# Optimization experiments

Hardware: AMD Instinct MI355X
Metric: run time of the kernel (lower is better)

Reference implementation:

```python
import jax, jax.numpy as jnp
import numpy as np

EMBED_DIM = 1024
NUM_HEADS = 16
HEAD_DIM = EMBED_DIM // NUM_HEADS
WINDOW = 256


def setup_inputs() -> dict:
    key = jax.random.key(0)
    ks = jax.random.split(key, 9)
    B, S, E = 4, 4096, EMBED_DIM
    sc = 1.0 / np.sqrt(E)
    return {
        "x": jax.random.normal(ks[0], (B, S, E), jnp.float32),
        "Wq": jax.random.normal(ks[1], (E, E), jnp.float32) * sc,
        "bq": jax.random.normal(ks[2], (E,), jnp.float32) * 0.01,
        "Wk": jax.random.normal(ks[3], (E, E), jnp.float32) * sc,
        "bk": jax.random.normal(ks[4], (E,), jnp.float32) * 0.01,
        "Wv": jax.random.normal(ks[5], (E, E), jnp.float32) * sc,
        "bv": jax.random.normal(ks[6], (E,), jnp.float32) * 0.01,
        "Wo": jax.random.normal(ks[7], (E, E), jnp.float32) * sc,
        "bo": jax.random.normal(ks[8], (E,), jnp.float32) * 0.01,
    }


def reference(x, Wq, bq, Wk, bk, Wv, bv, Wo, bo):
    B, S, E = x.shape
    H, D, W = NUM_HEADS, HEAD_DIM, WINDOW
    NW = S // W  # seq_len chosen divisible by window -> no padding

    def split_heads(t):  # [B,S,E] -> [B,H,NW,W,D]
        return t.reshape(B, S, H, D).transpose(0, 2, 1, 3).reshape(B, H, NW, W, D)

    q = split_heads(x @ Wq + bq)
    k = split_heads(x @ Wk + bk)
    v = split_heads(x @ Wv + bv)

    # block-diagonal attention within each non-overlapping window
    scores = jnp.einsum("bhnqd,bhnkd->bhnqk", q, k) / jnp.sqrt(
        jnp.asarray(D, x.dtype))
    attn = jax.nn.softmax(scores, axis=-1)
    out = jnp.einsum("bhnqk,bhnkd->bhnqd", attn, v)  # [B,H,NW,W,D]

    out = out.reshape(B, H, S, D).transpose(0, 2, 1, 3).reshape(B, S, E)
    return out @ Wo + bo
```

## Files before the change

### kernel.cpp

```cpp
#include <hip/hip_runtime.h>

typedef __bf16 bf16x8 __attribute__((ext_vector_type(8)));
typedef float  f32x4  __attribute__((ext_vector_type(4)));

#define MFMA(a,b,c) __builtin_amdgcn_mfma_f32_16x16x32_bf16((a),(b),(c),0,0,0)
#define VMC(N) asm volatile("s_waitcnt vmcnt(" #N ")" ::: "memory")

__device__ __forceinline__ unsigned short f2bf(float f){
  unsigned u = __builtin_bit_cast(unsigned, f);
  u += 0x7fffu + ((u>>16)&1u);
  return (unsigned short)(u>>16);
}
__device__ __forceinline__ unsigned pack_bf2(float a, float b){
  return (unsigned)f2bf(a) | ((unsigned)f2bf(b)<<16);
}
__device__ __forceinline__ void gload_lds16(const void* g, void* l){
  __builtin_amdgcn_global_load_lds((__attribute__((address_space(1))) void*)(g),
                                   (__attribute__((address_space(3))) void*)(l), 16, 0, 0);
}

__global__ void k_cvt_x(const float* __restrict__ x, unsigned short* __restrict__ o){
  const size_t t = (size_t)blockIdx.x*256 + threadIdx.x;
  #pragma unroll
  for (int i=0;i<4;i++){
    size_t idx = t + (size_t)i*1048576;
    float4 f = ((const float4*)x)[idx];
    ((uint2*)o)[idx] = make_uint2(pack_bf2(f.x,f.y), pack_bf2(f.z,f.w));
  }
}

__global__ void k_cvt_wT(const float* __restrict__ Wq, const float* __restrict__ Wk,
                         const float* __restrict__ Wv, const float* __restrict__ Wo,
                         unsigned short* __restrict__ wT){
  const int z = blockIdx.z;
  const float* W = (z==0)?Wq:(z==1)?Wk:(z==2)?Wv:Wo;
  unsigned short* out = wT + (size_t)z*1048576;
  __shared__ float tile[32][33];
  const int r0 = blockIdx.y*32, c0 = blockIdx.x*32;
  const int r = threadIdx.x>>5, c = threadIdx.x&31;
  #pragma unroll
  for (int i=0;i<4;i++) tile[r + i*8][c] = W[(size_t)(r0 + r + i*8)*1024 + c0 + c];
  __syncthreads();
  #pragma unroll
  for (int i=0;i<4;i++)
    out[(size_t)(c0 + r + i*8)*1024 + r0 + c] = f2bf(tile[c][r + i*8]);
}

#define QUAD16(AF, BF, MF0) do { \
  _Pragma("unroll") \
  for (int mf_=0; mf_<4; ++mf_){ \
    _Pragma("unroll") \
    for (int nf_=0; nf_<4; ++nf_) \
      acc[MF0+mf_][nf_] = MFMA(AF[mf_], BF[nf_], acc[MF0+mf_][nf_]); \
  } } while(0)

#define RDA(DST, MF0, P) do { \
  _Pragma("unroll") \
  for (int mf_=0; mf_<4; ++mf_) \
    DST[mf_] = *(const bf16x8*)((P) + ((MF0)+mf_)*2048); \
  } while(0)

#define RDB(DST, P) do { \
  _Pragma("unroll") \
  for (int nf_=0; nf_<4; ++nf_) \
    DST[nf_] = *(const bf16x8*)((P) + nf_*2048); \
  } while(0)

#define STG2(P0, P1, DT, ISA, BUF, HF) do { \
  char* _ld = smem + ((ISA)?0:65536) + (BUF)*32768 + (HF)*16384 + wid*1024; \
  gload_lds16((P0) + (DT), _ld); \
  gload_lds16((P1) + (DT), _ld + 8192); \
  } while(0)

#define PH_OPEN   __builtin_amdgcn_s_barrier(); __builtin_amdgcn_s_setprio(1)
#define PH_CLOSE  __builtin_amdgcn_s_setprio(0)
#define PH_END    __builtin_amdgcn_s_barrier()

template<int MODE>
__global__ __launch_bounds__(512,2) void k_gemm8(const unsigned short* __restrict__ A,
                       const unsigned short* __restrict__ Bm,
                       const float* __restrict__ bias0, const float* __restrict__ bias1,
                       const float* __restrict__ bias2,
                       unsigned short* __restrict__ q_ws, unsigned short* __restrict__ k_ws,
                       unsigned short* __restrict__ v_ws, float* __restrict__ outf)
{
  __shared__ char smem[131072];
  const int tid = threadIdx.x, lane = tid&63, wid = tid>>6;
  const int g = lane>>4, l15 = lane&15;
  const int wr = wid>>2, wc = wid&3;

  constexpr int NN = (MODE==0)? 12 : 4;
  const int x  = blockIdx.x & 7;
  const int c  = blockIdx.x >> 3;
  const int m0 = ((c/NN)*8 + x) << 8;
  const int n0 = (c%NN) << 8;

  f32x4 acc[8][4];
  #pragma unroll
  for (int i=0;i<8;i++)
    #pragma unroll
    for (int j=0;j<4;j++) acc[i][j] = f32x4{0.f,0.f,0.f,0.f};

  const int sw = (l15&7)<<4;
  const int brow = (wc&1)*64;

  const char* dsA00 = smem + wr*16384 + l15*128 + ((g*16) ^ sw);
  const char* dsA01 = smem + wr*16384 + l15*128 + ((64+g*16) ^ sw);
  const char* dsA10 = dsA00 + 32768;
  const char* dsA11 = dsA01 + 32768;
  const char* dsB00 = smem + 65536 + (wc>>1)*16384 + (brow+l15)*128 + ((g*16) ^ sw);
  const char* dsB01 = smem + 65536 + (wc>>1)*16384 + (brow+l15)*128 + ((64+g*16) ^ sw);
  const char* dsB10 = dsB00 + 32768;
  const char* dsB11 = dsB01 + 32768;

  const int rj = tid>>3;
  const int cs = ((tid*16)&127) ^ ((rj&7)<<4);
  const char* pgA0_0 = (const char*)A  + (size_t)(m0 +       rj)*2048 + cs;
  const char* pgA0_1 = (const char*)A  + (size_t)(m0 +  64 + rj)*2048 + cs;
  const char* pgA1_0 = (const char*)A  + (size_t)(m0 + 128 + rj)*2048 + cs;
  const char* pgA1_1 = (const char*)A  + (size_t)(m0 + 192 + rj)*2048 + cs;
  const char* pgB0_0 = (const char*)Bm + (size_t)(n0 +       rj)*2048 + cs;
  const char* pgB0_1 = (const char*)Bm + (size_t)(n0 +  64 + rj)*2048 + cs;
  const char* pgB1_0 = (const char*)Bm + (size_t)(n0 + 128 + rj)*2048 + cs;
  const char* pgB1_1 = (const char*)Bm + (size_t)(n0 + 192 + rj)*2048 + cs;

  bf16x8 aF[4], bF[4];

  STG2(pgA0_0, pgA0_1, 0, 1, 0, 0);
  STG2(pgA1_0, pgA1_1, 0, 1, 0, 1);
  STG2(pgB0_0, pgB0_1, 0, 0, 0, 0);
  STG2(pgB1_0, pgB1_1, 0, 0, 0, 1);
  STG2(pgB0_0, pgB0_1, 128, 0, 1, 0);
  VMC(2);
  __builtin_amdgcn_s_barrier();

  #pragma unroll 1
  for (int i=0;i<7;++i){
    RDA(aF,0,dsA00); RDB(bF,dsB00); STG2(pgB1_0,pgB1_1,128,0,1,1);
    PH_OPEN; QUAD16(aF,bF,0); PH_CLOSE; PH_END;
    RDA(aF,4,dsA00); STG2(pgA0_0,pgA0_1,128,1,1,0);
    PH_OPEN; QUAD16(aF,bF,4); PH_CLOSE; PH_END;
    RDA(aF,0,dsA01); RDB(bF,dsB01); STG2(pgA1_0,pgA1_1,128,1,1,1);
    PH_OPEN; QUAD16(aF,bF,0); PH_CLOSE; PH_END;
    RDA(aF,4,dsA01); STG2(pgB0_0,pgB0_1,256,0,0,0);
    PH_OPEN; QUAD16(aF,bF,4); PH_CLOSE; VMC(2); PH_END;
    RDA(aF,0,dsA10); RDB(bF,dsB10); STG2(pgB1_0,pgB1_1,256,0,0,1);
    PH_OPEN; QUAD16(aF,bF,0); PH_CLOSE; PH_END;
    RDA(aF,4,dsA10); STG2(pgA0_0,pgA0_1,256,1,0,0);
    PH_OPEN; QUAD16(aF,bF,4); PH_CLOSE; PH_END;
    RDA(aF,0,dsA11); RDB(bF,dsB11); STG2(pgA1_0,pgA1_1,256,1,0,1);
    PH_OPEN; QUAD16(aF,bF,0); PH_CLOSE; PH_END;
    RDA(aF,4,dsA11); STG2(pgB0_0,pgB0_1,384,0,1,0);
    PH_OPEN; QUAD16(aF,bF,4); PH_CLOSE; VMC(2); PH_END;
    pgA0_0 += 256; pgA0_1 += 256; pgA1_0 += 256; pgA1_1 += 256;
    pgB0_0 += 256; pgB0_1 += 256; pgB1_0 += 256; pgB1_1 += 256;
  }
  {
    RDA(aF,0,dsA00); RDB(bF,dsB00); STG2(pgB1_0,pgB1_1,128,0,1,1);
    PH_OPEN; QUAD16(aF,bF,0); PH_CLOSE; PH_END;
    RDA(aF,4,dsA00); STG2(pgA0_0,pgA0_1,128,1,1,0);
    PH_OPEN; QUAD16(aF,bF,4); PH_CLOSE; PH_END;
    RDA(aF,0,dsA01); RDB(bF,dsB01); STG2(pgA1_0,pgA1_1,128,1,1,1);
    PH_OPEN; QUAD16(aF,bF,0); PH_CLOSE; PH_END;
    RDA(aF,4,dsA01);
    PH_OPEN; QUAD16(aF,bF,4); PH_CLOSE; VMC(0); PH_END;
    RDA(aF,0,dsA10); RDB(bF,dsB10);
    PH_OPEN; QUAD16(aF,bF,0); PH_CLOSE; PH_END;
    RDA(aF,4,dsA10);
    PH_OPEN; QUAD16(aF,bF,4); PH_CLOSE; PH_END;
    RDA(aF,0,dsA11); RDB(bF,dsB11);
    PH_OPEN; QUAD16(aF,bF,0); PH_CLOSE; PH_END;
    RDA(aF,4,dsA11);
    PH_OPEN; QUAD16(aF,bF,4); PH_CLOSE; PH_END;
  }

  if constexpr (MODE==0){
    const int z  = n0>>10;
    const int nE = n0 & 1023;
    const float* bias = (z==0)? bias0 : (z==1)? bias1 : bias2;
    #pragma unroll
    for (int nf=0;nf<4;nf++){
      const int ncol = nE + wc*64 + nf*16 + l15;
      const float bn = bias[ncol];
      const int h = ncol>>6, d = ncol&63;
      #pragma unroll
      for (int mf=0;mf<8;mf++){
        const int mb = m0 + wr*128 + mf*16 + g*4;
        if (z==2){
          const int b = mb>>12, s = mb&4095, nw = s>>8, w0 = s&255;
          unsigned short pk0=f2bf(acc[mf][nf][0]+bn), pk1=f2bf(acc[mf][nf][1]+bn),
                         pk2=f2bf(acc[mf][nf][2]+bn), pk3=f2bf(acc[mf][nf][3]+bn);
          size_t idx = ((((size_t)(b*16+h)*16 + nw)*64 + d)<<8) + w0;
          *(ushort4*)(v_ws + idx) = make_ushort4(pk0,pk1,pk2,pk3);
        } else {
          unsigned short* dst = (z==0)? q_ws : k_ws;
          const float scale = (z==0)? 0.125f : 1.0f;
          #pragma unroll
          for (int r=0;r<4;r++){
            const int m = mb + r, b = m>>12, s = m&4095;
            dst[(((size_t)(b*16+h)*4096 + s)<<6) + d] = f2bf((acc[mf][nf][r]+bn)*scale);
          }
        }
      }
    }
  } else {
    #pragma unroll
    for (int nf=0;nf<4;nf++){
      const int n = n0 + wc*64 + nf*16 + l15;
      const float bn = bias0[n];
      #pragma unroll
      for (int mf=0;mf<8;mf++)
        #pragma unroll
        for (int r=0;r<4;r++){
          const int m = m0 + wr*128 + mf*16 + g*4 + r;
          outf[(size_t)m*1024 + n] = acc[mf][nf][r] + bn;
        }
    }
  }
}

__global__ __launch_bounds__(256,2) void k_attn(const unsigned short* __restrict__ qw,
                                                const unsigned short* __restrict__ kw,
                                                const unsigned short* __restrict__ vw,
                                                unsigned short* __restrict__ ow)
{
  __shared__ unsigned short Ks[2][4096];
  __shared__ unsigned short Vs[2][4096];
  __shared__ unsigned short Ps[4][4096];
  const int tid = threadIdx.x, lane = tid&63, wid = tid>>6;
  const int g = lane>>4, l15 = lane&15;
  const int bhn = blockIdx.x;
  const int nw = bhn&15, h = (bhn>>4)&15, b = bhn>>8;

  const size_t qkbase = ((size_t)((b*16+h)*4096 + nw*256))<<6;
  const unsigned short* Qg = qw + qkbase;
  const unsigned short* Kg = kw + qkbase;
  const unsigned short* Vg = vw + (((size_t)(b*16+h)*16 + nw)<<14);
  const float NEG_INF = -__builtin_inff();

  bf16x8 qa[4][2];
  #pragma unroll
  for (int qf=0;qf<4;qf++)
    #pragma unroll
    for (int ks=0;ks<2;ks++)
      qa[qf][ks] = *(const bf16x8*)((const char*)Qg + (wid*64 + qf*16 + l15)*128 + ks*64 + g*16);

  auto stage = [&](int kt, int bi){
    #pragma unroll
    for (int i=0;i<4;i++){
      const int chunk = wid*4 + i;
      const int obase = (chunk&7)<<10;
      const int o = obase + lane*16;
      const int r = o>>7, cb = o&127;
      const int cs = cb ^ ((r&7)<<4);
      if (chunk < 8)
        gload_lds16((const char*)Kg + (kt*64 + r)*128 + cs, (char*)Ks[bi] + obase);
      else
        gload_lds16((const char*)Vg + r*512 + kt*128 + cs, (char*)Vs[bi] + obase);
    }
  };

  f32x4 oacc[4][4];
  float mrow[4][4], lrow[4][4];
  #pragma unroll
  for (int i=0;i<4;i++)
    #pragma unroll
    for (int j=0;j<4;j++){ oacc[i][j] = f32x4{0.f,0.f,0.f,0.f}; mrow[i][j] = NEG_INF; lrow[i][j] = 0.f; }

  stage(0,0);
  __syncthreads();
  for (int kt=0;kt<4;kt++){
    const int cur = kt&1;
    if (kt<3) stage(kt+1, cur^1);

    bf16x8 kb[4][2];
    #pragma unroll
    for (int kf=0;kf<4;kf++)
      #pragma unroll
      for (int ks=0;ks<2;ks++){
        const int kr = kf*16 + l15, cb = ks*64 + g*16;
        kb[kf][ks] = *(const bf16x8*)((const char*)Ks[cur] + kr*128 + (cb ^ ((kr&7)<<4)));
      }

    unsigned short* P = Ps[wid];
    #pragma unroll
    for (int qf=0;qf<4;qf++){
      f32x4 sfr[4];
      #pragma unroll
      for (int kf=0;kf<4;kf++){
        f32x4 zz = f32x4{0.f,0.f,0.f,0.f};
        zz = MFMA(qa[qf][0], kb[kf][0], zz);
        sfr[kf] = MFMA(qa[qf][1], kb[kf][1], zz);
      }
      #pragma unroll
      for (int r=0;r<4;r++){
        float t = fmaxf(fmaxf(sfr[0][r],sfr[1][r]), fmaxf(sfr[2][r],sfr[3][r]));
        t = fmaxf(t, __shfl_xor(t,1,64)); t = fmaxf(t, __shfl_xor(t,2,64));
        t = fmaxf(t, __shfl_xor(t,4,64)); t = fmaxf(t, __shfl_xor(t,8,64));
        const float mo = mrow[qf][r];
        const float mn = fmaxf(mo, t);
        const float alpha = __expf(mo - mn);
        float rs = 0.f;
        #pragma unroll
        for (int kf=0;kf<4;kf++){ float p = __expf(sfr[kf][r]-mn); sfr[kf][r] = p; rs += p; }
        rs += __shfl_xor(rs,1,64); rs += __shfl_xor(rs,2,64);
        rs += __shfl_xor(rs,4,64); rs += __shfl_xor(rs,8,64);
        lrow[qf][r] = lrow[qf][r]*alpha + rs;
        mrow[qf][r] = mn;
        #pragma unroll
        for (int df=0;df<4;df++) oacc[qf][df][r] *= alpha;
        const int prow = qf*16 + g*4 + r;
        const int sw = (prow&7)<<4;
        char* Pb = (char*)P + prow*128;
        #pragma unroll
        for (int kf=0;kf<4;kf++)
          *(unsigned short*)(Pb + (((kf*16 + l15)*2) ^ sw)) = f2bf(sfr[kf][r]);
      }
    }
    __builtin_amdgcn_sched_barrier(0);

    bf16x8 vb[4][2];
    #pragma unroll
    for (int df=0;df<4;df++)
      #pragma unroll
      for (int ks=0;ks<2;ks++){
        const int d = df*16 + l15, cb = ks*64 + g*16;
        vb[df][ks] = *(const bf16x8*)((const char*)Vs[cur] + d*128 + (cb ^ ((d&7)<<4)));
      }
    #pragma unroll
    for (int qf=0;qf<4;qf++){
      const int pr = qf*16 + l15;
      const bf16x8 pa0 = *(const bf16x8*)((const char*)P + pr*128 + ((g*16)      ^ ((pr&7)<<4)));
      const bf16x8 pa1 = *(const bf16x8*)((const char*)P + pr*128 + ((64 + g*16) ^ ((pr&7)<<4)));
      #pragma unroll
      for (int df=0;df<4;df++){
        oacc[qf][df] = MFMA(pa0, vb[df][0], oacc[qf][df]);
        oacc[qf][df] = MFMA(pa1, vb[df][1], oacc[qf][df]);
      }
    }
    __syncthreads();
  }

  #pragma unroll
  for (int qf=0;qf<4;qf++)
    #pragma unroll
    for (int r=0;r<4;r++){
      const float inv = 1.f / lrow[qf][r];
      const int srow = nw*256 + wid*64 + qf*16 + g*4 + r;
      const size_t base = ((size_t)b*4096 + srow)*1024 + (size_t)h*64;
      #pragma unroll
      for (int df=0;df<4;df++)
        ow[base + df*16 + l15] = f2bf(oacc[qf][df][r]*inv);
    }
}

extern "C" void kernel_launch(void* const* d_in, const int* in_sizes, int n_in,
                              void* d_out, int out_size, void* d_ws, size_t ws_size,
                              hipStream_t stream)
{
  const float* x  = (const float*)d_in[0];
  const float* Wq = (const float*)d_in[1];
  const float* bq = (const float*)d_in[2];
  const float* Wk = (const float*)d_in[3];
  const float* bk = (const float*)d_in[4];
  const float* Wv = (const float*)d_in[5];
  const float* bv = (const float*)d_in[6];
  const float* Wo = (const float*)d_in[7];
  const float* bo = (const float*)d_in[8];
  float* out = (float*)d_out;

  char* ws = (char*)d_ws;
  unsigned short* xbf  = (unsigned short*)(ws);
  unsigned short* wT   = (unsigned short*)(ws + (size_t)32*1048576);
  unsigned short* q_ws = (unsigned short*)(ws + (size_t)40*1048576);
  unsigned short* k_ws = (unsigned short*)(ws + (size_t)72*1048576);
  unsigned short* v_ws = (unsigned short*)(ws + (size_t)104*1048576);
  unsigned short* obf  = xbf;

  k_cvt_x<<<4096,256,0,stream>>>(x, xbf);
  k_cvt_wT<<<dim3(32,32,4),256,0,stream>>>(Wq,Wk,Wv,Wo, wT);
  k_gemm8<0><<<768,512,0,stream>>>(xbf, wT, bq,bk,bv, q_ws,k_ws,v_ws, nullptr);
  k_attn<<<1024,256,0,stream>>>(q_ws,k_ws,v_ws, obf);
  k_gemm8<1><<<256,512,0,stream>>>(obf, wT + (size_t)3*1048576, bo,nullptr,nullptr,
                                   nullptr,nullptr,nullptr, out);
}
```

Baseline: 255.4 us.

## Loop QKV GEMM over three projections per block and merge conversion kernels

The QKV projection GEMM now launches 256 blocks. Each block iterates over the Q, K and V weight slices for the same output column range, running a bias/store epilogue after each and keeping the A tile's L2 locality inside one persistent block. This replaces 768 blocks that each computed one projection tile. The x conversion and weight-transpose kernels are merged into one launch to remove a kernel boundary. The per-block work triples and 256 blocks may underfill the GPU. The mid-loop epilogues also stall the software pipeline.

Measured after the change: 263.2 us. +3.1%, slower.

```diff
diff --git a/kernel.cpp b/kernel.cpp
--- a/kernel.cpp
+++ b/kernel.cpp
@@ -19,31 +19,34 @@
                                    (__attribute__((address_space(3))) void*)(l), 16, 0, 0);
 }
 
-__global__ void k_cvt_x(const float* __restrict__ x, unsigned short* __restrict__ o){
-  const size_t t = (size_t)blockIdx.x*256 + threadIdx.x;
-  #pragma unroll
-  for (int i=0;i<4;i++){
-    size_t idx = t + (size_t)i*1048576;
-    float4 f = ((const float4*)x)[idx];
-    ((uint2*)o)[idx] = make_uint2(pack_bf2(f.x,f.y), pack_bf2(f.z,f.w));
+__global__ void k_cvt(const float* __restrict__ x,
+                      const float* __restrict__ Wq, const float* __restrict__ Wk,
+                      const float* __restrict__ Wv, const float* __restrict__ Wo,
+                      unsigned short* __restrict__ xbf, unsigned short* __restrict__ wT){
+  __shared__ float tile[32][33];
+  const int bb = blockIdx.x;
+  if (bb < 4096){
+    const size_t t = (size_t)bb*256 + threadIdx.x;
+    #pragma unroll
+    for (int i=0;i<4;i++){
+      size_t idx = t + (size_t)i*1048576;
+      float4 f = ((const float4*)x)[idx];
+      ((uint2*)xbf)[idx] = make_uint2(pack_bf2(f.x,f.y), pack_bf2(f.z,f.w));
+    }
+  } else {
+    const int zz = bb - 4096;
+    const int z = zz>>10;
+    const float* W = (z==0)?Wq:(z==1)?Wk:(z==2)?Wv:Wo;
+    unsigned short* out = wT + (size_t)z*1048576;
+    const int r0 = ((zz>>5)&31)*32, c0 = (zz&31)*32;
+    const int r = threadIdx.x>>5, c = threadIdx.x&31;
+    #pragma unroll
+    for (int i=0;i<4;i++) tile[r + i*8][c] = W[(size_t)(r0 + r + i*8)*1024 + c0 + c];
+    __syncthreads();
+    #pragma unroll
+    for (int i=0;i<4;i++)
+      out[(size_t)(c0 + r + i*8)*1024 + r0 + c] = f2bf(tile[c][r + i*8]);
   }
-}
-
-__global__ void k_cvt_wT(const float* __restrict__ Wq, const float* __restrict__ Wk,
-                         const float* __restrict__ Wv, const float* __restrict__ Wo,
-                         unsigned short* __restrict__ wT){
-  const int z = blockIdx.z;
-  const float* W = (z==0)?Wq:(z==1)?Wk:(z==2)?Wv:Wo;
-  unsigned short* out = wT + (size_t)z*1048576;
-  __shared__ float tile[32][33];
-  const int r0 = blockIdx.y*32, c0 = blockIdx.x*32;
-  const int r = threadIdx.x>>5, c = threadIdx.x&31;
-  #pragma unroll
-  for (int i=0;i<4;i++) tile[r + i*8][c] = W[(size_t)(r0 + r + i*8)*1024 + c0 + c];
-  __syncthreads();
-  #pragma unroll
-  for (int i=0;i<4;i++)
-    out[(size_t)(c0 + r + i*8)*1024 + r0 + c] = f2bf(tile[c][r + i*8]);
 }
 
 #define QUAD16(AF, BF, MF0) do { \
@@ -75,6 +78,9 @@
 #define PH_OPEN   __builtin_amdgcn_s_barrier(); __builtin_amdgcn_s_setprio(1)
 #define PH_CLOSE  __builtin_amdgcn_s_setprio(0)
 #define PH_END    __builtin_amdgcn_s_barrier()
+
+#define TB(u) ((((u)>>4)*2097152) + (((u)&15)<<7))
+#define TA(u) (((u)&15)<<7)
 
 template<int MODE>
 __global__ __launch_bounds__(512,2) void k_gemm8(const unsigned short* __restrict__ A,
@@ -89,11 +95,11 @@
   const int g = lane>>4, l15 = lane&15;
   const int wr = wid>>2, wc = wid&3;
 
-  constexpr int NN = (MODE==0)? 12 : 4;
+  constexpr int NZ = (MODE==0)? 3 : 1;
   const int x  = blockIdx.x & 7;
   const int c  = blockIdx.x >> 3;
-  const int m0 = ((c/NN)*8 + x) << 8;
-  const int n0 = (c%NN) << 8;
+  const int m0 = ((c>>2)*8 + x) << 8;
+  const int nE = (c&3) << 8;
 
   f32x4 acc[8][4];
   #pragma unroll
@@ -119,48 +125,93 @@
   const char* pgA0_1 = (const char*)A  + (size_t)(m0 +  64 + rj)*2048 + cs;
   const char* pgA1_0 = (const char*)A  + (size_t)(m0 + 128 + rj)*2048 + cs;
   const char* pgA1_1 = (const char*)A  + (size_t)(m0 + 192 + rj)*2048 + cs;
-  const char* pgB0_0 = (const char*)Bm + (size_t)(n0 +       rj)*2048 + cs;
-  const char* pgB0_1 = (const char*)Bm + (size_t)(n0 +  64 + rj)*2048 + cs;
-  const char* pgB1_0 = (const char*)Bm + (size_t)(n0 + 128 + rj)*2048 + cs;
-  const char* pgB1_1 = (const char*)Bm + (size_t)(n0 + 192 + rj)*2048 + cs;
+  const char* pgB0_0 = (const char*)Bm + (size_t)(nE +       rj)*2048 + cs;
+  const char* pgB0_1 = (const char*)Bm + (size_t)(nE +  64 + rj)*2048 + cs;
+  const char* pgB1_0 = (const char*)Bm + (size_t)(nE + 128 + rj)*2048 + cs;
+  const char* pgB1_1 = (const char*)Bm + (size_t)(nE + 192 + rj)*2048 + cs;
 
   bf16x8 aF[4], bF[4];
 
-  STG2(pgA0_0, pgA0_1, 0, 1, 0, 0);
-  STG2(pgA1_0, pgA1_1, 0, 1, 0, 1);
-  STG2(pgB0_0, pgB0_1, 0, 0, 0, 0);
-  STG2(pgB1_0, pgB1_1, 0, 0, 0, 1);
-  STG2(pgB0_0, pgB0_1, 128, 0, 1, 0);
+  auto epi = [&](int z){
+    if constexpr (MODE==0){
+      const float* bias = (z==0)? bias0 : (z==1)? bias1 : bias2;
+      if (z==2){
+        #pragma unroll
+        for (int nf=0;nf<4;nf++){
+          const int ncol = nE + wc*64 + nf*16 + l15;
+          const float bn = bias[ncol];
+          const int h = ncol>>6, d = ncol&63;
+          #pragma unroll
+          for (int mf=0;mf<8;mf++){
+            const int mb = m0 + wr*128 + mf*16 + g*4;
+            const int b = mb>>12, s = mb&4095, nw = s>>8, w0 = s&255;
+            unsigned short pk0=f2bf(acc[mf][nf][0]+bn), pk1=f2bf(acc[mf][nf][1]+bn),
+                           pk2=f2bf(acc[mf][nf][2]+bn), pk3=f2bf(acc[mf][nf][3]+bn);
+            size_t idx = ((((size_t)(b*16+h)*16 + nw)*64 + d)<<8) + w0;
+            *(ushort4*)(v_ws + idx) = make_ushort4(pk0,pk1,pk2,pk3);
+          }
+        }
+      } else {
+        unsigned short* dst = (z==0)? q_ws : k_ws;
+        const float scale = (z==0)? 0.125f : 1.0f;
+        #pragma unroll
+        for (int nf=0;nf<4;nf++){
+          const int ncol = nE + wc*64 + nf*16 + l15;
+          const float bn = bias[ncol];
+          const int h = ncol>>6, d = ncol&63;
+          #pragma unroll
+          for (int mf=0;mf<8;mf++){
+            const int mb = m0 + wr*128 + mf*16 + g*4;
+            #pragma unroll
+            for (int r=0;r<4;r++){
+              const int m = mb + r, b = m>>12, s = m&4095;
+              dst[(((size_t)(b*16+h)*4096 + s)<<6) + d] = f2bf((acc[mf][nf][r]+bn)*scale);
+            }
+          }
+        }
+      }
+      #pragma unroll
+      for (int i=0;i<8;i++)
+        #pragma unroll
+        for (int j=0;j<4;j++) acc[i][j] = f32x4{0.f,0.f,0.f,0.f};
+    }
+  };
+
+  STG2(pgA0_0, pgA0_1, TA(0), 1, 0, 0);
+  STG2(pgA1_0, pgA1_1, TA(0), 1, 0, 1);
+  STG2(pgB0_0, pgB0_1, TB(0), 0, 0, 0);
+  STG2(pgB1_0, pgB1_1, TB(0), 0, 0, 1);
+  STG2(pgB0_0, pgB0_1, TB(1), 0, 1, 0);
   VMC(2);
   __builtin_amdgcn_s_barrier();
 
   #pragma unroll 1
-  for (int i=0;i<7;++i){
-    RDA(aF,0,dsA00); RDB(bF,dsB00); STG2(pgB1_0,pgB1_1,128,0,1,1);
-    PH_OPEN; QUAD16(aF,bF,0); PH_CLOSE; PH_END;
-    RDA(aF,4,dsA00); STG2(pgA0_0,pgA0_1,128,1,1,0);
+  for (int j=0;j<8*NZ-1;++j){
+    const int T = 2*j;
+    RDA(aF,0,dsA00); RDB(bF,dsB00); STG2(pgB1_0,pgB1_1,TB(T+1),0,1,1);
+    PH_OPEN; QUAD16(aF,bF,0); PH_CLOSE; PH_END;
+    RDA(aF,4,dsA00); STG2(pgA0_0,pgA0_1,TA(T+1),1,1,0);
     PH_OPEN; QUAD16(aF,bF,4); PH_CLOSE; PH_END;
-    RDA(aF,0,dsA01); RDB(bF,dsB01); STG2(pgA1_0,pgA1_1,128,1,1,1);
-    PH_OPEN; QUAD16(aF,bF,0); PH_CLOSE; PH_END;
-    RDA(aF,4,dsA01); STG2(pgB0_0,pgB0_1,256,0,0,0);
+    RDA(aF,0,dsA01); RDB(bF,dsB01); STG2(pgA1_0,pgA1_1,TA(T+1),1,1,1);
+    PH_OPEN; QUAD16(aF,bF,0); PH_CLOSE; PH_END;
+    RDA(aF,4,dsA01); STG2(pgB0_0,pgB0_1,TB(T+2),0,0,0);
     PH_OPEN; QUAD16(aF,bF,4); PH_CLOSE; VMC(2); PH_END;
-    RDA(aF,0,dsA10); RDB(bF,dsB10); STG2(pgB1_0,pgB1_1,256,0,0,1);
-    PH_OPEN; QUAD16(aF,bF,0); PH_CLOSE; PH_END;
-    RDA(aF,4,dsA10); STG2(pgA0_0,pgA0_1,256,1,0,0);
+    RDA(aF,0,dsA10); RDB(bF,dsB10); STG2(pgB1_0,pgB1_1,TB(T+2),0,0,1);
+    PH_OPEN; QUAD16(aF,bF,0); PH_CLOSE; PH_END;
+    RDA(aF,4,dsA10); STG2(pgA0_0,pgA0_1,TA(T+2),1,0,0);
     PH_OPEN; QUAD16(aF,bF,4); PH_CLOSE; PH_END;
-    RDA(aF,0,dsA11); RDB(bF,dsB11); STG2(pgA1_0,pgA1_1,256,1,0,1);
-    PH_OPEN; QUAD16(aF,bF,0); PH_CLOSE; PH_END;
-    RDA(aF,4,dsA11); STG2(pgB0_0,pgB0_1,384,0,1,0);
+    RDA(aF,0,dsA11); RDB(bF,dsB11); STG2(pgA1_0,pgA1_1,TA(T+2),1,0,1);
+    PH_OPEN; QUAD16(aF,bF,0); PH_CLOSE; PH_END;
+    RDA(aF,4,dsA11); STG2(pgB0_0,pgB0_1,TB(T+3),0,1,0);
     PH_OPEN; QUAD16(aF,bF,4); PH_CLOSE; VMC(2); PH_END;
-    pgA0_0 += 256; pgA0_1 += 256; pgA1_0 += 256; pgA1_1 += 256;
-    pgB0_0 += 256; pgB0_1 += 256; pgB1_0 += 256; pgB1_1 += 256;
+    if (MODE==0 && (j&7)==7) epi(j>>3);
   }
   {
-    RDA(aF,0,dsA00); RDB(bF,dsB00); STG2(pgB1_0,pgB1_1,128,0,1,1);
-    PH_OPEN; QUAD16(aF,bF,0); PH_CLOSE; PH_END;
-    RDA(aF,4,dsA00); STG2(pgA0_0,pgA0_1,128,1,1,0);
+    RDA(aF,0,dsA00); RDB(bF,dsB00); STG2(pgB1_0,pgB1_1,TB(16*NZ-1),0,1,1);
+    PH_OPEN; QUAD16(aF,bF,0); PH_CLOSE; PH_END;
+    RDA(aF,4,dsA00); STG2(pgA0_0,pgA0_1,TA(16*NZ-1),1,1,0);
     PH_OPEN; QUAD16(aF,bF,4); PH_CLOSE; PH_END;
-    RDA(aF,0,dsA01); RDB(bF,dsB01); STG2(pgA1_0,pgA1_1,128,1,1,1);
+    RDA(aF,0,dsA01); RDB(bF,dsB01); STG2(pgA1_0,pgA1_1,TA(16*NZ-1),1,1,1);
     PH_OPEN; QUAD16(aF,bF,0); PH_CLOSE; PH_END;
     RDA(aF,4,dsA01);
     PH_OPEN; QUAD16(aF,bF,4); PH_CLOSE; VMC(0); PH_END;
@@ -175,38 +226,11 @@
   }
 
   if constexpr (MODE==0){
-    const int z  = n0>>10;
-    const int nE = n0 & 1023;
-    const float* bias = (z==0)? bias0 : (z==1)? bias1 : bias2;
+    epi(2);
+  } else {
     #pragma unroll
     for (int nf=0;nf<4;nf++){
-      const int ncol = nE + wc*64 + nf*16 + l15;
-      const float bn = bias[ncol];
-      const int h = ncol>>6, d = ncol&63;
-      #pragma unroll
-      for (int mf=0;mf<8;mf++){
-        const int mb = m0 + wr*128 + mf*16 + g*4;
-        if (z==2){
-          const int b = mb>>12, s = mb&4095, nw = s>>8, w0 = s&255;
-          unsigned short pk0=f2bf(acc[mf][nf][0]+bn), pk1=f2bf(acc[mf][nf][1]+bn),
-                         pk2=f2bf(acc[mf][nf][2]+bn), pk3=f2bf(acc[mf][nf][3]+bn);
-          size_t idx = ((((size_t)(b*16+h)*16 + nw)*64 + d)<<8) + w0;
-          *(ushort4*)(v_ws + idx) = make_ushort4(pk0,pk1,pk2,pk3);
-        } else {
-          unsigned short* dst = (z==0)? q_ws : k_ws;
-          const float scale = (z==0)? 0.125f : 1.0f;
-          #pragma unroll
-          for (int r=0;r<4;r++){
-            const int m = mb + r, b = m>>12, s = m&4095;
-            dst[(((size_t)(b*16+h)*4096 + s)<<6) + d] = f2bf((acc[mf][nf][r]+bn)*scale);
-          }
-        }
-      }
-    }
-  } else {
-    #pragma unroll
-    for (int nf=0;nf<4;nf++){
-      const int n = n0 + wc*64 + nf*16 + l15;
+      const int n = nE + wc*64 + nf*16 + l15;
       const float bn = bias0[n];
       #pragma unroll
       for (int mf=0;mf<8;mf++)
@@ -377,9 +401,8 @@
   unsigned short* v_ws = (unsigned short*)(ws + (size_t)104*1048576);
   unsigned short* obf  = xbf;
 
-  k_cvt_x<<<4096,256,0,stream>>>(x, xbf);
-  k_cvt_wT<<<dim3(32,32,4),256,0,stream>>>(Wq,Wk,Wv,Wo, wT);
-  k_gemm8<0><<<768,512,0,stream>>>(xbf, wT, bq,bk,bv, q_ws,k_ws,v_ws, nullptr);
+  k_cvt<<<8192,256,0,stream>>>(x, Wq,Wk,Wv,Wo, xbf, wT);
+  k_gemm8<0><<<256,512,0,stream>>>(xbf, wT, bq,bk,bv, q_ws,k_ws,v_ws, nullptr);
   k_attn<<<1024,256,0,stream>>>(q_ws,k_ws,v_ws, obf);
   k_gemm8<1><<<256,512,0,stream>>>(obf, wT + (size_t)3*1048576, bo,nullptr,nullptr,
                                    nullptr,nullptr,nullptr, out);
```
